# Kernel tuning notes

Hardware: AMD Instinct MI355X
Metric: run time of the kernel (lower is better)

Reference implementation:

```python
import jax, jax.numpy as jnp
import numpy as np
import itertools

DIM = 576; HEADS = 18; HD = 32; WS = 7; H = 28; W = 28; EPS = 1e-5

def _bias_idxs(ws):
    pts = list(itertools.product(range(ws), range(ws)))
    offs = {}
    idxs = []
    for p1 in pts:
        for p2 in pts:
            o = (abs(p1[0] - p2[0]), abs(p1[1] - p2[1]))
            if o not in offs:
                offs[o] = len(offs)
            idxs.append(offs[o])
    return np.array(idxs, np.int32).reshape(len(pts), len(pts))

BIAS_IDXS = _bias_idxs(WS)          # [49, 49]
N_OFF = int(BIAS_IDXS.max()) + 1    # 49 distinct offsets

def _ln(x, g, b):
    m = x.mean(-1, keepdims=True)
    v = ((x - m) ** 2).mean(-1, keepdims=True)
    return (x - m) * jax.lax.rsqrt(v + EPS) * g + b

def setup_inputs() -> dict:
    key = jax.random.key(0)
    ks = jax.random.split(key, 10)
    B = 32; L = H * W; C = DIM; hid = 4 * C
    s = 0.02
    return {
        'x': jax.random.normal(ks[0], (B, L, C), jnp.float32),
        'ln1_g': jnp.ones((C,), jnp.float32),
        'ln1_b': jnp.zeros((C,), jnp.float32),
        'qkv_w': jax.random.normal(ks[1], (C, 3 * C), jnp.float32) * s,
        'qkv_b': jnp.zeros((3 * C,), jnp.float32),
        'attn_biases': jax.random.normal(ks[2], (HEADS, N_OFF), jnp.float32) * s,
        'proj_w': jax.random.normal(ks[3], (C, C), jnp.float32) * s,
        'proj_b': jnp.zeros((C,), jnp.float32),
        'conv_w': jax.random.normal(ks[4], (C, 1, 3, 3), jnp.float32) * 0.1,
        'bn_g': jnp.ones((C,), jnp.float32),
        'bn_b': jnp.zeros((C,), jnp.float32),
        'bn_mean': jax.random.normal(ks[5], (C,), jnp.float32) * 0.1,
        'bn_var': jax.random.uniform(ks[6], (C,), jnp.float32, 0.5, 1.5),
        'ln2_g': jnp.ones((C,), jnp.float32),
        'ln2_b': jnp.zeros((C,), jnp.float32),
        'fc1_w': jax.random.normal(ks[7], (C, hid), jnp.float32) * s,
        'fc1_b': jnp.zeros((hid,), jnp.float32),
        'fc2_w': jax.random.normal(ks[8], (hid, C), jnp.float32) * s,
        'fc2_b': jnp.zeros((C,), jnp.float32),
    }

def reference(x, ln1_g, ln1_b, qkv_w, qkv_b, attn_biases, proj_w, proj_b,
              conv_w, bn_g, bn_b, bn_mean, bn_var, ln2_g, ln2_b,
              fc1_w, fc1_b, fc2_w, fc2_b):
    B, L, C = x.shape
    nH, nW = H // WS, W // WS
    Nw = WS * WS
    scale = HD ** -0.5
    res = x
    # window partition: [B,L,C] -> [B*nH*nW, WS*WS, C] (H,W divisible by WS -> no pad)
    xw = x.reshape(B, nH, WS, nW, WS, C).transpose(0, 1, 3, 2, 4, 5).reshape(-1, Nw, C)
    h = _ln(xw, ln1_g, ln1_b)
    qkv = (h @ qkv_w + qkv_b).reshape(-1, Nw, HEADS, 3 * HD)
    q, k, v = qkv[..., :HD], qkv[..., HD:2 * HD], qkv[..., 2 * HD:]
    bias = attn_biases[:, BIAS_IDXS]  # gather -> [HEADS, Nw, Nw]
    scores = jnp.einsum('bnhd,bmhd->bhnm', q, k) * scale + bias[None]
    a = jax.nn.softmax(scores, axis=-1)
    o = jnp.einsum('bhnm,bmhd->bnhd', a, v).reshape(-1, Nw, C)
    o = o @ proj_w + proj_b
    # window reverse
    o = o.reshape(B, nH, nW, WS, WS, C).transpose(0, 1, 3, 2, 4, 5).reshape(B, L, C)
    x = res + o
    # depthwise 3x3 conv + BatchNorm (eval mode, running stats)
    xc = x.transpose(0, 2, 1).reshape(B, C, H, W)
    y = jax.lax.conv_general_dilated(xc, conv_w, (1, 1), ((1, 1), (1, 1)),
                                     feature_group_count=C,
                                     dimension_numbers=('NCHW', 'OIHW', 'NCHW'))
    inv = jax.lax.rsqrt(bn_var + EPS)
    y = (y - bn_mean[None, :, None, None]) * (inv * bn_g)[None, :, None, None] + bn_b[None, :, None, None]
    x = y.reshape(B, C, L).transpose(0, 2, 1)
    # MLP with pre-LayerNorm (exact GELU, matching torch nn.GELU)
    hm = _ln(x, ln2_g, ln2_b)
    hm = jax.nn.gelu(hm @ fc1_w + fc1_b, approximate=False)
    x = x + (hm @ fc2_w + fc2_b)
    return x
```

## Files before the change

### kernel.cpp

```cpp
#include <hip/hip_runtime.h>
#include <hip/hip_bf16.h>

typedef __attribute__((ext_vector_type(8))) short bf16x8;
typedef __attribute__((ext_vector_type(4))) float f32x4;

static __device__ __forceinline__ void stf(float* p, size_t i, float v) { p[i] = v; }
static __device__ __forceinline__ void stf(__hip_bfloat16* p, size_t i, float v) { p[i] = __float2bfloat16(v); }

static __device__ __forceinline__ void gload_lds16(const void* g, void* l) {
  __builtin_amdgcn_global_load_lds((const __attribute__((address_space(1))) void*)g,
                                   (__attribute__((address_space(3))) void*)l, 16, 0, 0);
}

__global__ void wt_kernel(const float* __restrict__ W, __hip_bfloat16* __restrict__ WT, int K, int N) {
  __shared__ float tile[32][33];
  const int kb = blockIdx.y * 32, nb = blockIdx.x * 32;
  const int tx = threadIdx.x & 31, ty = threadIdx.x >> 5;
#pragma unroll
  for (int i = 0; i < 4; ++i)
    tile[ty + i * 8][tx] = W[(size_t)(kb + ty + i * 8) * N + nb + tx];
  __syncthreads();
#pragma unroll
  for (int i = 0; i < 4; ++i)
    WT[(size_t)(nb + ty + i * 8) * K + kb + tx] = __float2bfloat16(tile[tx][ty + i * 8]);
}

__global__ void convprep_kernel(const float* __restrict__ w, const float* __restrict__ bng,
                                const float* __restrict__ bnb, const float* __restrict__ bnm,
                                const float* __restrict__ bnv, float* __restrict__ wT,
                                float* __restrict__ st) {
  const int i = blockIdx.x * 256 + threadIdx.x;
  if (i < 576 * 9) {
    const int t = i / 576, c = i - t * 576;
    wT[i] = w[c * 9 + t];
  }
  if (i < 576) {
    const float s = rsqrtf(bnv[i] + 1e-5f) * bng[i];
    st[i] = s;
    st[576 + i] = bnb[i] - bnm[i] * s;
  }
}

__global__ void ln_bf16_kernel(const float* __restrict__ x, const float* __restrict__ g,
                               const float* __restrict__ b, __hip_bfloat16* __restrict__ y) {
  const int row = blockIdx.x * 4 + (threadIdx.x >> 6);
  const int lane = threadIdx.x & 63;
  const float* p = x + (size_t)row * 576;
  float vals[9];
  float s = 0.f, ss = 0.f;
#pragma unroll
  for (int i = 0; i < 9; ++i) {
    float v = p[lane + i * 64];
    vals[i] = v; s += v; ss += v * v;
  }
#pragma unroll
  for (int o = 32; o; o >>= 1) { s += __shfl_down(s, o); ss += __shfl_down(ss, o); }
  s = __shfl(s, 0); ss = __shfl(ss, 0);
  const float m = s * (1.f / 576.f);
  const float rstd = rsqrtf(ss * (1.f / 576.f) - m * m + 1e-5f);
  __hip_bfloat16* q = y + (size_t)row * 576;
#pragma unroll
  for (int i = 0; i < 9; ++i) {
    const int c = lane + i * 64;
    q[c] = __float2bfloat16((vals[i] - m) * rstd * g[c] + b[c]);
  }
}

template <int BM, int BN, int EPI, typename TO>
__global__ __launch_bounds__(256, 2) void gemm_bt(
    const __hip_bfloat16* __restrict__ A, const __hip_bfloat16* __restrict__ BT,
    const float* __restrict__ bias, const float* __restrict__ res, TO* __restrict__ C,
    int M, int N, int K) {
  constexpr int WM = BM / 2, WN = BN / 2;
  constexpr int MI = WM / 16, NI = WN / 16;
  constexpr int AI = BM / 32, BI = BN / 32;
  __shared__ __hip_bfloat16 sA[2][BM * 64];
  __shared__ __hip_bfloat16 sB[2][BN * 64];
  const int t = threadIdx.x;
  const int lane = t & 63;
  const int w = t >> 6;
  const int nwg = gridDim.x;
  const int qq = nwg >> 3, r = nwg & 7;
  const int xcd = blockIdx.x & 7, lidx = blockIdx.x >> 3;
  const int wgid = (xcd < r ? xcd * (qq + 1) : r * (qq + 1) + (xcd - r) * qq) + lidx;
  const int nx = N / BN;
  const int bm = (wgid / nx) * BM, bn = (wgid % nx) * BN;
  const int wm = (w >> 1) * WM, wn = (w & 1) * WN;
  const int l15 = lane & 15, l4 = lane >> 4;

  f32x4 acc[MI][NI];
#pragma unroll
  for (int mi = 0; mi < MI; ++mi)
#pragma unroll
    for (int ni = 0; ni < NI; ++ni) acc[mi][ni] = (f32x4){0.f, 0.f, 0.f, 0.f};

  const int wave_base = t & ~63;

  auto stage = [&](int buf, int k0) {
#pragma unroll
    for (int i = 0; i < AI; ++i) {
      const int slot = i * 256 + t;
      const int row = slot >> 3, kst = slot & 7;
      const int ksrc = kst ^ (row & 7);
      const __hip_bfloat16* g = A + (size_t)(bm + row) * K + k0 + ksrc * 8;
      gload_lds16(g, sA[buf] + (i * 256 + wave_base) * 8);
    }
#pragma unroll
    for (int i = 0; i < BI; ++i) {
      const int slot = i * 256 + t;
      const int row = slot >> 3, kst = slot & 7;
      const int ksrc = kst ^ (row & 7);
      const __hip_bfloat16* g = BT + (size_t)(bn + row) * K + k0 + ksrc * 8;
      gload_lds16(g, sB[buf] + (i * 256 + wave_base) * 8);
    }
  };

  auto compute = [&](int buf) {
    const __hip_bfloat16* pA = sA[buf];
    const __hip_bfloat16* pB = sB[buf];
#pragma unroll
    for (int kb = 0; kb < 2; ++kb) {
      bf16x8 a[MI], b[NI];
      const int kblk = kb * 4 + l4;
#pragma unroll
      for (int mi = 0; mi < MI; ++mi) {
        const int row = wm + mi * 16 + l15;
        a[mi] = *(const bf16x8*)(pA + row * 64 + ((kblk ^ (row & 7)) * 8));
      }
#pragma unroll
      for (int ni = 0; ni < NI; ++ni) {
        const int row = wn + ni * 16 + l15;
        b[ni] = *(const bf16x8*)(pB + row * 64 + ((kblk ^ (row & 7)) * 8));
      }
#pragma unroll
      for (int mi = 0; mi < MI; ++mi)
#pragma unroll
        for (int ni = 0; ni < NI; ++ni)
          acc[mi][ni] = __builtin_amdgcn_mfma_f32_16x16x32_bf16(a[mi], b[ni], acc[mi][ni], 0, 0, 0);
    }
  };

  const int nt = K >> 6;
  stage(0, 0);
  __syncthreads();
  int cur = 0;
  for (int tt = 0; tt < nt - 1; ++tt) {
    stage(cur ^ 1, (tt + 1) << 6);
    compute(cur);
    __syncthreads();
    cur ^= 1;
  }
  compute(cur);

#pragma unroll
  for (int mi = 0; mi < MI; ++mi) {
    const int mrow = bm + wm + mi * 16 + l4 * 4;
#pragma unroll
    for (int ni = 0; ni < NI; ++ni) {
      const int col = bn + wn + ni * 16 + l15;
      const float bv = bias[col];
#pragma unroll
      for (int r2 = 0; r2 < 4; ++r2) {
        const size_t idx = (size_t)(mrow + r2) * N + col;
        float v = acc[mi][ni][r2] + bv;
        if (EPI == 1) v += res[idx];
        if (EPI == 2) v = 0.5f * v * (1.0f + erff(v * 0.70710678118654752f));
        stf(C, idx, v);
      }
    }
  }
}

__global__ __launch_bounds__(64) void attn_mfma_kernel(
    const __hip_bfloat16* __restrict__ qkv, const float* __restrict__ biases,
    __hip_bfloat16* __restrict__ o) {
  __shared__ __hip_bfloat16 sQK[2][64][40];
  __shared__ __hip_bfloat16 sVT[32][72];
  __hip_bfloat16 (*sP)[72] = (__hip_bfloat16(*)[72])(&sQK[0][0][0]);

  const int wid  = blockIdx.x / 18;
  const int head = blockIdx.x - wid * 18;
  const int b  = wid >> 4;
  const int wi = wid & 15;
  const int wh = wi >> 2, wwc = wi & 3;
  const int lane = threadIdx.x;
  const int l15 = lane & 15, l4 = lane >> 4;

  {
    const __hip_bfloat16* basep = qkv + (size_t)head * 96;
    for (int idx = lane; idx < 49 * 12; idx += 64) {
      const int tkn = idx / 12, part = idx - tkn * 12;
      const int r = tkn / 7, c = tkn - r * 7;
      const size_t row = (size_t)b * 784 + (size_t)((wh * 7 + r) * 28 + wwc * 7 + c);
      bf16x8 v = *(const bf16x8*)(basep + row * 1728 + part * 8);
      if (part < 4)      *(bf16x8*)&sQK[0][tkn][part * 8] = v;
      else if (part < 8) *(bf16x8*)&sQK[1][tkn][(part - 4) * 8] = v;
      else {
        const int d0 = (part - 8) * 8;
        const short* sv = (const short*)&v;
#pragma unroll
        for (int e = 0; e < 8; ++e)
          sVT[d0 + e][tkn] = *(const __hip_bfloat16*)&sv[e];
      }
    }
    for (int idx = lane; idx < 32 * 15; idx += 64) {
      const int d = idx / 15, tt = 49 + (idx - d * 15);
      sVT[d][tt] = __float2bfloat16(0.0f);
    }
  }
  __syncthreads();

  f32x4 acc[4][4];
#pragma unroll
  for (int mi = 0; mi < 4; ++mi)
#pragma unroll
    for (int ni = 0; ni < 4; ++ni) acc[mi][ni] = (f32x4){0.f, 0.f, 0.f, 0.f};
  {
    bf16x8 aq[4], bk[4];
#pragma unroll
    for (int mi = 0; mi < 4; ++mi) aq[mi] = *(const bf16x8*)&sQK[0][mi * 16 + l15][l4 * 8];
#pragma unroll
    for (int ni = 0; ni < 4; ++ni) bk[ni] = *(const bf16x8*)&sQK[1][ni * 16 + l15][l4 * 8];
#pragma unroll
    for (int mi = 0; mi < 4; ++mi)
#pragma unroll
      for (int ni = 0; ni < 4; ++ni)
        acc[mi][ni] = __builtin_amdgcn_mfma_f32_16x16x32_bf16(aq[mi], bk[ni], acc[mi][ni], 0, 0, 0);
  }
  __syncthreads();

  const float scale = 0.17677669529663687f;
  const float* btab = biases + head * 49;
#pragma unroll
  for (int mi = 0; mi < 4; ++mi) {
#pragma unroll
    for (int rr = 0; rr < 4; ++rr) {
      const int i = mi * 16 + l4 * 4 + rr;
      const int ic = i < 49 ? i : 0;
      const int ri = ic / 7, ci = ic - ri * 7;
      float s[4];
#pragma unroll
      for (int ni = 0; ni < 4; ++ni) {
        const int j = ni * 16 + l15;
        if (j < 49) {
          const int rj = j / 7, cj = j - rj * 7;
          s[ni] = acc[mi][ni][rr] * scale + btab[__builtin_abs(ri - rj) * 7 + __builtin_abs(ci - cj)];
        } else {
          s[ni] = -1e30f;
        }
      }
      float m = fmaxf(fmaxf(s[0], s[1]), fmaxf(s[2], s[3]));
#pragma unroll
      for (int d = 1; d < 16; d <<= 1) m = fmaxf(m, __shfl_xor(m, d));
      float sum = 0.f;
#pragma unroll
      for (int ni = 0; ni < 4; ++ni) { s[ni] = __expf(s[ni] - m); sum += s[ni]; }
#pragma unroll
      for (int d = 1; d < 16; d <<= 1) sum += __shfl_xor(sum, d);
      const float inv = 1.0f / sum;
#pragma unroll
      for (int ni = 0; ni < 4; ++ni)
        sP[i][ni * 16 + l15] = __float2bfloat16(s[ni] * inv);
    }
  }
  __syncthreads();

  f32x4 oacc[4][2];
#pragma unroll
  for (int mi = 0; mi < 4; ++mi)
#pragma unroll
    for (int ni = 0; ni < 2; ++ni) oacc[mi][ni] = (f32x4){0.f, 0.f, 0.f, 0.f};
#pragma unroll
  for (int kb = 0; kb < 2; ++kb) {
    bf16x8 ap[4], bv[2];
#pragma unroll
    for (int mi = 0; mi < 4; ++mi) ap[mi] = *(const bf16x8*)&sP[mi * 16 + l15][kb * 32 + l4 * 8];
#pragma unroll
    for (int ni = 0; ni < 2; ++ni) bv[ni] = *(const bf16x8*)&sVT[ni * 16 + l15][kb * 32 + l4 * 8];
#pragma unroll
    for (int mi = 0; mi < 4; ++mi)
#pragma unroll
      for (int ni = 0; ni < 2; ++ni)
        oacc[mi][ni] = __builtin_amdgcn_mfma_f32_16x16x32_bf16(ap[mi], bv[ni], oacc[mi][ni], 0, 0, 0);
  }

#pragma unroll
  for (int mi = 0; mi < 4; ++mi) {
#pragma unroll
    for (int rr = 0; rr < 4; ++rr) {
      const int i = mi * 16 + l4 * 4 + rr;
      if (i < 49) {
        const int r = i / 7, c = i - r * 7;
        const size_t grow = (size_t)b * 784 + (size_t)((wh * 7 + r) * 28 + wwc * 7 + c);
#pragma unroll
        for (int ni = 0; ni < 2; ++ni)
          o[grow * 576 + head * 32 + ni * 16 + l15] = __float2bfloat16(oacc[mi][ni][rr]);
      }
    }
  }
}

__global__ void conv_bn_kernel(const float* __restrict__ x1, const float* __restrict__ wT,
                               const float* __restrict__ st, float* __restrict__ x2) {
  const size_t total = (size_t)32 * 784 * 144;
  const size_t idx = (size_t)blockIdx.x * 256 + threadIdx.x;
  if (idx >= total) return;
  const int c4 = (int)(idx % 144);
  const size_t p = idx / 144;
  const int pix = (int)(p % 784);
  const int b = (int)(p / 784);
  const int i = pix / 28, j = pix - (pix / 28) * 28;
  const int c = c4 * 4;
  f32x4 acc = (f32x4){0.f, 0.f, 0.f, 0.f};
#pragma unroll
  for (int dh = -1; dh <= 1; ++dh) {
#pragma unroll
    for (int dw = -1; dw <= 1; ++dw) {
      const int ii = i + dh, jj = j + dw;
      if (ii >= 0 && ii < 28 && jj >= 0 && jj < 28) {
        const f32x4 v = *(const f32x4*)&x1[((size_t)b * 784 + ii * 28 + jj) * 576 + c];
        const f32x4 wv = *(const f32x4*)&wT[((dh + 1) * 3 + (dw + 1)) * 576 + c];
        acc += v * wv;
      }
    }
  }
  const f32x4 s = *(const f32x4*)&st[c];
  const f32x4 tt = *(const f32x4*)&st[576 + c];
  *(f32x4*)&x2[((size_t)b * 784 + pix) * 576 + c] = acc * s + tt;
}

extern "C" void kernel_launch(void* const* d_in, const int* in_sizes, int n_in,
                              void* d_out, int out_size, void* d_ws, size_t ws_size,
                              hipStream_t stream) {
  (void)in_sizes; (void)n_in; (void)out_size; (void)ws_size;
  const float* x      = (const float*)d_in[0];
  const float* ln1g   = (const float*)d_in[1];
  const float* ln1b   = (const float*)d_in[2];
  const float* qkv_w  = (const float*)d_in[3];
  const float* qkv_b  = (const float*)d_in[4];
  const float* biases = (const float*)d_in[5];
  const float* proj_w = (const float*)d_in[6];
  const float* proj_b = (const float*)d_in[7];
  const float* conv_w = (const float*)d_in[8];
  const float* bng    = (const float*)d_in[9];
  const float* bnb    = (const float*)d_in[10];
  const float* bnm    = (const float*)d_in[11];
  const float* bnv    = (const float*)d_in[12];
  const float* ln2g   = (const float*)d_in[13];
  const float* ln2b   = (const float*)d_in[14];
  const float* fc1_w  = (const float*)d_in[15];
  const float* fc1_b  = (const float*)d_in[16];
  const float* fc2_w  = (const float*)d_in[17];
  const float* fc2_b  = (const float*)d_in[18];
  float* out = (float*)d_out;

  const int M = 25088;
  char* ws = (char*)d_ws;
  float* x2 = (float*)ws;
  char* regB = ws + 57802752;
  __hip_bfloat16* qkvb = (__hip_bfloat16*)regB;
  float*          x1   = (float*)regB;
  __hip_bfloat16* hm   = (__hip_bfloat16*)regB;
  char* regC = ws + 173408256;
  __hip_bfloat16* xn1  = (__hip_bfloat16*)regC;
  __hip_bfloat16* obuf = (__hip_bfloat16*)regC;
  __hip_bfloat16* xn2  = (__hip_bfloat16*)regC;
  char* regD = ws + 202309632;
  __hip_bfloat16* qkvT = (__hip_bfloat16*)regD;
  __hip_bfloat16* projT = (__hip_bfloat16*)(regD + 1990656);
  __hip_bfloat16* fc1T  = (__hip_bfloat16*)(regD + 1990656 + 663552);
  __hip_bfloat16* fc2T  = (__hip_bfloat16*)(regD + 1990656 + 663552 + 2654208);
  float* convT = (float*)(ws + 210272256);
  float* convST = convT + 9 * 576;

  wt_kernel<<<dim3(1728 / 32, 576 / 32), 256, 0, stream>>>(qkv_w, qkvT, 576, 1728);
  wt_kernel<<<dim3(576 / 32, 576 / 32), 256, 0, stream>>>(proj_w, projT, 576, 576);
  wt_kernel<<<dim3(2304 / 32, 576 / 32), 256, 0, stream>>>(fc1_w, fc1T, 576, 2304);
  wt_kernel<<<dim3(576 / 32, 2304 / 32), 256, 0, stream>>>(fc2_w, fc2T, 2304, 576);
  convprep_kernel<<<(576 * 9 + 255) / 256, 256, 0, stream>>>(conv_w, bng, bnb, bnm, bnv, convT, convST);

  ln_bf16_kernel<<<M / 4, 256, 0, stream>>>(x, ln1g, ln1b, xn1);
  gemm_bt<128, 192, 0, __hip_bfloat16><<<9 * 196, 256, 0, stream>>>(xn1, qkvT, qkv_b, nullptr, qkvb, M, 1728, 576);
  attn_mfma_kernel<<<512 * 18, 64, 0, stream>>>(qkvb, biases, obuf);
  gemm_bt<128, 192, 1, float><<<3 * 196, 256, 0, stream>>>(obuf, projT, proj_b, x, x1, M, 576, 576);
  conv_bn_kernel<<<(32 * 784 * 144 + 255) / 256, 256, 0, stream>>>(x1, convT, convST, x2);
  ln_bf16_kernel<<<M / 4, 256, 0, stream>>>(x2, ln2g, ln2b, xn2);
  gemm_bt<128, 192, 2, __hip_bfloat16><<<12 * 196, 256, 0, stream>>>(xn2, fc1T, fc1_b, nullptr, hm, M, 2304, 576);
  gemm_bt<128, 192, 1, float><<<3 * 196, 256, 0, stream>>>(hm, fc2T, fc2_b, x2, out, M, 576, 2304);
}
```

Before: 555.5 us.

## Enlarge GEMM tile to 256x192 with 8 waves and deeper prefetch pipeline

The GEMM moves to a fixed 256x192 block tile computed by 512 threads (8 waves in a 2x4 grid, each wave doing 128x48). It also replaces the simple double-buffer loop with a two-tile-ahead prefetch that uses explicit vmcnt waits and raw s_barriers, so global-to-LDS loads overlap compute more fully. The bigger tile raises operand reuse and halves the number of workgroups. In exchange, each wave holds many more accumulator registers (24 MFMA tiles) and occupancy drops to one block per CU. The hardcoded vmcnt(7) count is fragile because it must match the 7 loads issued per stage.

Result: no change. 561.8 us (+1.1%).

```diff
diff --git a/kernel.cpp b/kernel.cpp
--- a/kernel.cpp
+++ b/kernel.cpp
@@ -66,14 +66,15 @@
   }
 }
 
-template <int BM, int BN, int EPI, typename TO>
-__global__ __launch_bounds__(256, 2) void gemm_bt(
+template <int EPI, typename TO>
+__global__ __launch_bounds__(512, 1) void gemm_bt(
     const __hip_bfloat16* __restrict__ A, const __hip_bfloat16* __restrict__ BT,
     const float* __restrict__ bias, const float* __restrict__ res, TO* __restrict__ C,
     int M, int N, int K) {
-  constexpr int WM = BM / 2, WN = BN / 2;
-  constexpr int MI = WM / 16, NI = WN / 16;
-  constexpr int AI = BM / 32, BI = BN / 32;
+  constexpr int BM = 256, BN = 192;
+  constexpr int WM = 128, WN = 48;
+  constexpr int MI = 8, NI = 3;
+  constexpr int AI = 4, BI = 3;
   __shared__ __hip_bfloat16 sA[2][BM * 64];
   __shared__ __hip_bfloat16 sB[2][BN * 64];
   const int t = threadIdx.x;
@@ -85,7 +86,7 @@
   const int wgid = (xcd < r ? xcd * (qq + 1) : r * (qq + 1) + (xcd - r) * qq) + lidx;
   const int nx = N / BN;
   const int bm = (wgid / nx) * BM, bn = (wgid % nx) * BN;
-  const int wm = (w >> 1) * WM, wn = (w & 1) * WN;
+  const int wm = (w >> 2) * WM, wn = (w & 3) * WN;
   const int l15 = lane & 15, l4 = lane >> 4;
 
   f32x4 acc[MI][NI];
@@ -96,22 +97,23 @@
 
   const int wave_base = t & ~63;
 
-  auto stage = [&](int buf, int k0) {
+  auto stage = [&](int buf, int kt) {
+    const int k0 = kt << 6;
 #pragma unroll
     for (int i = 0; i < AI; ++i) {
-      const int slot = i * 256 + t;
+      const int slot = i * 512 + t;
       const int row = slot >> 3, kst = slot & 7;
       const int ksrc = kst ^ (row & 7);
       const __hip_bfloat16* g = A + (size_t)(bm + row) * K + k0 + ksrc * 8;
-      gload_lds16(g, sA[buf] + (i * 256 + wave_base) * 8);
+      gload_lds16(g, sA[buf] + (i * 512 + wave_base) * 8);
     }
 #pragma unroll
     for (int i = 0; i < BI; ++i) {
-      const int slot = i * 256 + t;
+      const int slot = i * 512 + t;
       const int row = slot >> 3, kst = slot & 7;
       const int ksrc = kst ^ (row & 7);
       const __hip_bfloat16* g = BT + (size_t)(bn + row) * K + k0 + ksrc * 8;
-      gload_lds16(g, sB[buf] + (i * 256 + wave_base) * 8);
+      gload_lds16(g, sB[buf] + (i * 512 + wave_base) * 8);
     }
   };
 
@@ -142,15 +144,23 @@
 
   const int nt = K >> 6;
   stage(0, 0);
-  __syncthreads();
+  stage(1, 1);
   int cur = 0;
-  for (int tt = 0; tt < nt - 1; ++tt) {
-    stage(cur ^ 1, (tt + 1) << 6);
+  for (int tt = 0; tt < nt; ++tt) {
+    if (tt < nt - 1) asm volatile("s_waitcnt vmcnt(7)" ::: "memory");
+    else             asm volatile("s_waitcnt vmcnt(0)" ::: "memory");
+    __builtin_amdgcn_sched_barrier(0);
+    __builtin_amdgcn_s_barrier();
+    __builtin_amdgcn_sched_barrier(0);
     compute(cur);
-    __syncthreads();
+    if (tt + 2 < nt) {
+      __builtin_amdgcn_sched_barrier(0);
+      __builtin_amdgcn_s_barrier();
+      __builtin_amdgcn_sched_barrier(0);
+      stage(cur, tt + 2);
+    }
     cur ^= 1;
   }
-  compute(cur);
 
 #pragma unroll
   for (int mi = 0; mi < MI; ++mi) {
@@ -380,11 +390,11 @@
   convprep_kernel<<<(576 * 9 + 255) / 256, 256, 0, stream>>>(conv_w, bng, bnb, bnm, bnv, convT, convST);
 
   ln_bf16_kernel<<<M / 4, 256, 0, stream>>>(x, ln1g, ln1b, xn1);
-  gemm_bt<128, 192, 0, __hip_bfloat16><<<9 * 196, 256, 0, stream>>>(xn1, qkvT, qkv_b, nullptr, qkvb, M, 1728, 576);
+  gemm_bt<0, __hip_bfloat16><<<98 * 9, 512, 0, stream>>>(xn1, qkvT, qkv_b, nullptr, qkvb, M, 1728, 576);
   attn_mfma_kernel<<<512 * 18, 64, 0, stream>>>(qkvb, biases, obuf);
-  gemm_bt<128, 192, 1, float><<<3 * 196, 256, 0, stream>>>(obuf, projT, proj_b, x, x1, M, 576, 576);
+  gemm_bt<1, float><<<98 * 3, 512, 0, stream>>>(obuf, projT, proj_b, x, x1, M, 576, 576);
   conv_bn_kernel<<<(32 * 784 * 144 + 255) / 256, 256, 0, stream>>>(x1, convT, convST, x2);
   ln_bf16_kernel<<<M / 4, 256, 0, stream>>>(x2, ln2g, ln2b, xn2);
-  gemm_bt<128, 192, 2, __hip_bfloat16><<<12 * 196, 256, 0, stream>>>(xn2, fc1T, fc1_b, nullptr, hm, M, 2304, 576);
-  gemm_bt<128, 192, 1, float><<<3 * 196, 256, 0, stream>>>(hm, fc2T, fc2_b, x2, out, M, 576, 2304);
-}
+  gemm_bt<2, __hip_bfloat16><<<98 * 12, 512, 0, stream>>>(xn2, fc1T, fc1_b, nullptr, hm, M, 2304, 576);
+  gemm_bt<1, float><<<98 * 3, 512, 0, stream>>>(hm, fc2T, fc2_b, x2, out, M, 576, 2304);
+}
```
